# Kernel optimization log

Hardware: AMD Instinct MI355X
Metric: run time of the kernel (lower is better)

## Reference

```python
import jax, jax.numpy as jnp
import numpy as np

N_EDGES = 1600000
N_NODES = 50000
D_FEAT = 48


def setup_inputs() -> dict:
    key = jax.random.key(0)
    k1, k2, k3 = jax.random.split(key, 3)
    a = jax.random.normal(k1, (N_EDGES,), dtype=jnp.float32)
    ft = jax.random.normal(k2, (N_EDGES, D_FEAT), dtype=jnp.float32)
    segment_ids = jnp.sort(jax.random.randint(k3, (N_EDGES,), 0, N_NODES, dtype=jnp.int32))
    return {"a": a, "ft": ft, "segment_ids": segment_ids, "n_nodes": N_NODES}


def reference(a, ft, segment_ids, n_nodes):
    # Segment softmax over incoming edges of each destination node
    # (the torch module does softmax over the stacked neighbor-message axis).
    seg_max = jax.ops.segment_max(a, segment_ids, num_segments=n_nodes)  # [N]
    seg_max = jax.lax.stop_gradient(seg_max)  # stabilizer only, grad-neutral
    ex = jnp.exp(a - seg_max[segment_ids])                               # [E]
    denom = jax.ops.segment_sum(ex, segment_ids, num_segments=n_nodes)  # [N]
    e = ex / denom[segment_ids]                                         # [E]
    # Weighted sum of neighbor features per node: sum_e e * ft  -> [N, D]
    out = jax.ops.segment_sum(e[:, None] * ft, segment_ids, num_segments=n_nodes)
    return out
```

## Files before the change

### kernel.cpp

```cpp
#include <hip/hip_runtime.h>
#include <cfloat>
#include <cstdint>

#define D_FEAT 48

__global__ void build_rowptr(const int* __restrict__ seg, int E, int N,
                             int* __restrict__ row_ptr) {
    int e = blockIdx.x * blockDim.x + threadIdx.x;
    if (e >= E) return;
    int s  = seg[e];
    int sp = (e == 0) ? -1 : seg[e - 1];
    for (int n = sp + 1; n <= s; ++n) row_ptr[n] = e;
    if (e == E - 1) {
        for (int n = s + 1; n <= N; ++n) row_ptr[n] = E;
    }
}

__global__ __launch_bounds__(256) void gat_reduce(
    const float* __restrict__ a, const float* __restrict__ ft,
    const int* __restrict__ row_ptr, float* __restrict__ out, int N)
{
    int lane = threadIdx.x & 63;
    int n = blockIdx.x * 4 + (threadIdx.x >> 6);
    if (n >= N) return;

    int lo  = row_ptr[n];
    int hi  = row_ptr[n + 1];
    int cnt = hi - lo;

    if (cnt <= 0) {
        if (lane < D_FEAT) out[(size_t)n * D_FEAT + lane] = 0.0f;
        return;
    }

    float mx = -FLT_MAX;
    for (int i = lane; i < cnt; i += 64) mx = fmaxf(mx, a[lo + i]);
    #pragma unroll
    for (int o = 32; o > 0; o >>= 1) mx = fmaxf(mx, __shfl_xor(mx, o, 64));

    float s = 0.0f;
    for (int i = lane; i < cnt; i += 64) s += __expf(a[lo + i] - mx);
    #pragma unroll
    for (int o = 32; o > 0; o >>= 1) s += __shfl_xor(s, o, 64);
    float inv = 1.0f / s;

    float acc = 0.0f;
    const float* fp = ft + (size_t)lo * D_FEAT;
    for (int i = 0; i < cnt; ++i) {
        float w = __expf(a[lo + i] - mx) * inv;
        if (lane < D_FEAT) acc += w * fp[(size_t)i * D_FEAT + lane];
    }
    if (lane < D_FEAT) out[(size_t)n * D_FEAT + lane] = acc;
}

extern "C" void kernel_launch(void* const* d_in, const int* in_sizes, int n_in,
                              void* d_out, int out_size, void* d_ws, size_t ws_size,
                              hipStream_t stream) {
    const float* a   = (const float*)d_in[0];
    const float* ft  = (const float*)d_in[1];
    const int*   seg = (const int*)d_in[2];
    int E = in_sizes[0];
    int N = out_size / D_FEAT;

    int* row_ptr = (int*)d_ws;

    build_rowptr<<<(E + 255) / 256, 256, 0, stream>>>(seg, E, N, row_ptr);
    gat_reduce<<<(N + 3) / 4, 256, 0, stream>>>(a, ft, row_ptr, (float*)d_out, N);
}
```

Before: 497.1 us.

## Vectorize feature accumulation with float4 lanes processing four edges concurrently

```diff
diff --git a/kernel.cpp b/kernel.cpp
--- a/kernel.cpp
+++ b/kernel.cpp
@@ -28,8 +28,14 @@
     int hi  = row_ptr[n + 1];
     int cnt = hi - lo;
 
+    int m    = lane % 12;
+    int ecls = lane / 12;
+
     if (cnt <= 0) {
-        if (lane < D_FEAT) out[(size_t)n * D_FEAT + lane] = 0.0f;
+        if (lane < 12) {
+            float4 z = {0.f, 0.f, 0.f, 0.f};
+            *(float4*)(out + (size_t)n * D_FEAT + 4 * lane) = z;
+        }
         return;
     }
 
@@ -44,13 +50,49 @@
     for (int o = 32; o > 0; o >>= 1) s += __shfl_xor(s, o, 64);
     float inv = 1.0f / s;
 
-    float acc = 0.0f;
-    const float* fp = ft + (size_t)lo * D_FEAT;
-    for (int i = 0; i < cnt; ++i) {
-        float w = __expf(a[lo + i] - mx) * inv;
-        if (lane < D_FEAT) acc += w * fp[(size_t)i * D_FEAT + lane];
+    float4 acc = {0.f, 0.f, 0.f, 0.f};
+    if (lane < 48) {
+        const float* base = ft + (size_t)lo * D_FEAT + 4 * m;
+        const float* ap   = a + lo;
+        int ngroups = (cnt + 3) >> 2;
+        for (int g = 0; g < ngroups; g += 4) {
+            float4 f[4];
+            #pragma unroll
+            for (int k = 0; k < 4; ++k) {
+                int e  = (g + k) * 4 + ecls;
+                int ec = min(e, cnt - 1);
+                f[k] = *(const float4*)(base + (size_t)ec * D_FEAT);
+            }
+            float w[4];
+            #pragma unroll
+            for (int k = 0; k < 4; ++k) {
+                int e  = (g + k) * 4 + ecls;
+                int ec = min(e, cnt - 1);
+                float av = ap[ec];
+                w[k] = (e < cnt) ? __expf(av - mx) : 0.0f;
+            }
+            #pragma unroll
+            for (int k = 0; k < 4; ++k) {
+                acc.x = fmaf(w[k], f[k].x, acc.x);
+                acc.y = fmaf(w[k], f[k].y, acc.y);
+                acc.z = fmaf(w[k], f[k].z, acc.z);
+                acc.w = fmaf(w[k], f[k].w, acc.w);
+            }
+        }
     }
-    if (lane < D_FEAT) out[(size_t)n * D_FEAT + lane] = acc;
+
+    float4 t;
+    t.x = __shfl(acc.x, lane + 24, 64); t.y = __shfl(acc.y, lane + 24, 64);
+    t.z = __shfl(acc.z, lane + 24, 64); t.w = __shfl(acc.w, lane + 24, 64);
+    acc.x += t.x; acc.y += t.y; acc.z += t.z; acc.w += t.w;
+    t.x = __shfl(acc.x, lane + 12, 64); t.y = __shfl(acc.y, lane + 12, 64);
+    t.z = __shfl(acc.z, lane + 12, 64); t.w = __shfl(acc.w, lane + 12, 64);
+    acc.x += t.x; acc.y += t.y; acc.z += t.z; acc.w += t.w;
+
+    if (lane < 12) {
+        float4 r = {acc.x * inv, acc.y * inv, acc.z * inv, acc.w * inv};
+        *(float4*)(out + (size_t)n * D_FEAT + 4 * lane) = r;
+    }
 }
 
 extern "C" void kernel_launch(void* const* d_in, const int* in_sizes, int n_in,
```

After: 422.8 us. -14.9%, faster.
